# Optimization experiments

Hardware: AMD Instinct MI355X
Metric: run time of the kernel (lower is better)

## Reference

```python
import jax, jax.numpy as jnp
import numpy as np

B, S, D, R = 8, 2048, 2048, 256


def soft_threshold24(w):
    """2:4 soft-threshold: in each contiguous group of 4 along the last dim,
    keep the top-2 |w| and shrink them by the 3rd-largest |w| (soft threshold),
    zeroing the bottom two. Mirrors soft_threshold24_triton."""
    rows, K = w.shape
    g = w.reshape(rows, K // 4, 4)
    a = jnp.abs(g)
    t = jnp.sort(a, axis=-1)[..., 1:2]  # 2nd smallest == 3rd largest per group
    sp = jnp.sign(g) * jnp.maximum(a - t, 0.0)
    return sp.reshape(rows, K)


def fp16_mm(a, b):
    """fake_fp8_mm: cast operands to fp16, matmul with fp32 accumulation/output."""
    return jnp.matmul(a.astype(jnp.float16), b.astype(jnp.float16),
                      preferred_element_type=jnp.float32)


def sparse_linear(x, w, b, scale):
    """SparseOverlayFunction.forward: 2:4-sparsified, scaled weight + fp16 GEMM."""
    x2 = x.reshape(-1, x.shape[-1])                # [N, K]
    ws = soft_threshold24(w) * scale               # [K, M], 2:4 sparse * learnable scale
    out = fp16_mm(x2, ws)                          # [N, M] fp32
    out = out.reshape(x.shape[:-1] + (w.shape[-1],))
    return out + b


def setup_inputs():
    key = jax.random.key(0)
    ks = jax.random.split(key, 4)
    x = jax.random.normal(ks[0], (B, S, D), jnp.float32)
    weight_in = jax.random.normal(ks[1], (D, R), jnp.float32) * 0.02
    weight_out = jax.random.normal(ks[2], (R, D), jnp.float32) * 0.02
    bias_in = jnp.zeros((R,), jnp.float32)
    bias_out = jax.random.normal(ks[3], (D,), jnp.float32) * 0.01
    sparse_scale_in = jnp.ones((1,), jnp.float32)
    sparse_scale_out = jnp.ones((1,), jnp.float32)
    return {"x": x, "weight_in": weight_in, "weight_out": weight_out,
            "bias_in": bias_in, "bias_out": bias_out,
            "sparse_scale_in": sparse_scale_in, "sparse_scale_out": sparse_scale_out}


def reference(x, weight_in, weight_out, bias_in, bias_out, sparse_scale_in, sparse_scale_out):
    h = sparse_linear(x, weight_in, bias_in, sparse_scale_in)    # [B,S,R]
    y = sparse_linear(h, weight_out, bias_out, sparse_scale_out)  # [B,S,D]
    return y
```

## Files before the change

### kernel.cpp

```cpp
#include <hip/hip_runtime.h>
#include <stdint.h>
#include <stddef.h>

typedef _Float16 f16;
typedef __attribute__((ext_vector_type(8))) _Float16 f16x8;
typedef __attribute__((ext_vector_type(4))) float f32x4;

#define GPTR(p) ((const __attribute__((address_space(1))) void*)(p))
#define LPTR(p) ((__attribute__((address_space(3))) void*)(p))

__device__ __forceinline__ void async16(const void* g, void* l) {
    __builtin_amdgcn_global_load_lds(GPTR(g), LPTR(l), 16, 0, 0);
}

__global__ __launch_bounds__(256) void sparsify_t_tiled(
        const float* __restrict__ W, const float* __restrict__ scale,
        f16* __restrict__ Wt, int K, int M) {
    __shared__ f16 T[64][80];
    const int r0 = blockIdx.y << 6, m0 = blockIdx.x << 6;
    const float s = scale[0];
    const int t = threadIdx.x;
    const int rr = t >> 2, mb = (t & 3) << 4;
    const float* src = W + (size_t)(r0 + rr) * M + m0 + mb;
    #pragma unroll
    for (int j = 0; j < 4; j++) {
        float4 v = *(const float4*)(src + j * 4);
        float a0 = fabsf(v.x), a1 = fabsf(v.y), a2 = fabsf(v.z), a3 = fabsf(v.w);
        float lo1 = fminf(a0, a1), hi1 = fmaxf(a0, a1);
        float lo2 = fminf(a2, a3), hi2 = fmaxf(a2, a3);
        float th = fminf(fmaxf(lo1, lo2), fminf(hi1, hi2));
        int m = mb + j * 4;
        T[m + 0][rr] = (f16)(copysignf(fmaxf(a0 - th, 0.f), v.x) * s);
        T[m + 1][rr] = (f16)(copysignf(fmaxf(a1 - th, 0.f), v.y) * s);
        T[m + 2][rr] = (f16)(copysignf(fmaxf(a2 - th, 0.f), v.z) * s);
        T[m + 3][rr] = (f16)(copysignf(fmaxf(a3 - th, 0.f), v.w) * s);
    }
    __syncthreads();
    const int mm = t >> 2, rb = (t & 3) << 4;
    f16* dst = Wt + (size_t)(m0 + mm) * K + r0 + rb;
    *(f16x8*)dst       = *(const f16x8*)&T[mm][rb];
    *(f16x8*)(dst + 8) = *(const f16x8*)&T[mm][rb + 8];
}

__global__ __launch_bounds__(256, 4) void gemm1_kernel(
        const float* __restrict__ A, const f16* __restrict__ Bt,
        const float* __restrict__ bias, f16* __restrict__ H) {
    constexpr int K = 2048, RN = 256, BK = 64;
    __shared__ float4 Asf[64 * 16];
    __shared__ f16x8  Bs[64 * 8];

    const int tid  = threadIdx.x;
    const int lane = tid & 63;
    const int wv   = tid >> 6;
    const int wm   = wv & 1, wn = wv >> 1;
    const int lr   = lane & 15, q = lane >> 4;
    const int row0 = blockIdx.y << 6;
    const int col0 = blockIdx.x << 6;

    f32x4 acc[2][2] = {};

    for (int k0 = 0; k0 < K; k0 += BK) {
        #pragma unroll
        for (int j = 0; j < 4; j++) {
            int issue = wv * 4 + j;
            int L = issue * 64 + lane;
            int r = L >> 4, cp = L & 15;
            int c = (cp & 8) | ((cp & 7) ^ (r & 7));
            async16(A + (size_t)(row0 + r) * K + k0 + c * 4,
                    (char*)Asf + issue * 1024);
        }
        #pragma unroll
        for (int j = 0; j < 2; j++) {
            int issue = wv * 2 + j;
            int L = issue * 64 + lane;
            int r = L >> 3, cp = L & 7;
            int c = cp ^ (r & 7);
            async16(Bt + (size_t)(col0 + r) * K + k0 + c * 8,
                    (char*)Bs + issue * 1024);
        }
        __syncthreads();

        #pragma unroll
        for (int ks = 0; ks < 2; ks++) {
            f16x8 af[2], bf[2];
            #pragma unroll
            for (int m = 0; m < 2; m++) {
                int r = wm * 32 + m * 16 + lr;
                int c0p = ks * 8 + (((2 * q) + 0) ^ (r & 7));
                int c1p = ks * 8 + (((2 * q) + 1) ^ (r & 7));
                float4 v0 = Asf[r * 16 + c0p];
                float4 v1 = Asf[r * 16 + c1p];
                f16x8 h;
                h[0] = (f16)v0.x; h[1] = (f16)v0.y; h[2] = (f16)v0.z; h[3] = (f16)v0.w;
                h[4] = (f16)v1.x; h[5] = (f16)v1.y; h[6] = (f16)v1.z; h[7] = (f16)v1.w;
                af[m] = h;
            }
            #pragma unroll
            for (int n = 0; n < 2; n++) {
                int r = wn * 32 + n * 16 + lr;
                int cp = (ks * 4 + q) ^ (r & 7);
                bf[n] = Bs[r * 8 + cp];
            }
            #pragma unroll
            for (int m = 0; m < 2; m++)
                #pragma unroll
                for (int n = 0; n < 2; n++)
                    acc[m][n] = __builtin_amdgcn_mfma_f32_16x16x32_f16(
                        af[m], bf[n], acc[m][n], 0, 0, 0);
        }
        __syncthreads();
    }

    #pragma unroll
    for (int m = 0; m < 2; m++) {
        int gr0 = row0 + wm * 32 + m * 16 + q * 4;
        #pragma unroll
        for (int n = 0; n < 2; n++) {
            int gc = col0 + wn * 32 + n * 16 + lr;
            float bv = bias[gc];
            #pragma unroll
            for (int r = 0; r < 4; r++)
                H[(size_t)(gr0 + r) * RN + gc] = (f16)(acc[m][n][r] + bv);
        }
    }
}

__global__ __launch_bounds__(256, 4) void gemm2_kernel(
        const f16* __restrict__ H, const f16* __restrict__ Bt,
        const float* __restrict__ bias, float* __restrict__ Y) {
    constexpr int K = 256, N = 2048, BK = 64;
    __shared__ f16x8 As[64 * 8];
    __shared__ f16x8 Bs[128 * 8];

    const int tid  = threadIdx.x;
    const int lane = tid & 63;
    const int wv   = tid >> 6;
    const int wm   = wv & 1, wn = wv >> 1;
    const int lr   = lane & 15, q = lane >> 4;
    const int row0 = blockIdx.y << 6;
    const int col0 = blockIdx.x << 7;

    f32x4 acc[2][4] = {};

    for (int k0 = 0; k0 < K; k0 += BK) {
        #pragma unroll
        for (int j = 0; j < 2; j++) {
            int issue = wv * 2 + j;
            int L = issue * 64 + lane;
            int r = L >> 3, cp = L & 7;
            int c = cp ^ (r & 7);
            async16(H + (size_t)(row0 + r) * K + k0 + c * 8,
                    (char*)As + issue * 1024);
        }
        #pragma unroll
        for (int j = 0; j < 4; j++) {
            int issue = wv * 4 + j;
            int L = issue * 64 + lane;
            int r = L >> 3, cp = L & 7;
            int c = cp ^ (r & 7);
            async16(Bt + (size_t)(col0 + r) * K + k0 + c * 8,
                    (char*)Bs + issue * 1024);
        }
        __syncthreads();

        #pragma unroll
        for (int ks = 0; ks < 2; ks++) {
            f16x8 af[2], bf[4];
            #pragma unroll
            for (int m = 0; m < 2; m++) {
                int r = wm * 32 + m * 16 + lr;
                af[m] = As[r * 8 + ((ks * 4 + q) ^ (r & 7))];
            }
            #pragma unroll
            for (int n = 0; n < 4; n++) {
                int r = wn * 64 + n * 16 + lr;
                bf[n] = Bs[r * 8 + ((ks * 4 + q) ^ (r & 7))];
            }
            #pragma unroll
            for (int m = 0; m < 2; m++)
                #pragma unroll
                for (int n = 0; n < 4; n++)
                    acc[m][n] = __builtin_amdgcn_mfma_f32_16x16x32_f16(
                        af[m], bf[n], acc[m][n], 0, 0, 0);
        }
        __syncthreads();
    }

    #pragma unroll
    for (int m = 0; m < 2; m++) {
        int gr0 = row0 + wm * 32 + m * 16 + q * 4;
        #pragma unroll
        for (int n = 0; n < 4; n++) {
            int gc = col0 + wn * 64 + n * 16 + lr;
            float bv = bias[gc];
            #pragma unroll
            for (int r = 0; r < 4; r++)
                Y[(size_t)(gr0 + r) * N + gc] = acc[m][n][r] + bv;
        }
    }
}

extern "C" void kernel_launch(void* const* d_in, const int* in_sizes, int n_in,
                              void* d_out, int out_size, void* d_ws, size_t ws_size,
                              hipStream_t stream) {
    const float* x  = (const float*)d_in[0];
    const float* w1 = (const float*)d_in[1];
    const float* w2 = (const float*)d_in[2];
    const float* b1 = (const float*)d_in[3];
    const float* b2 = (const float*)d_in[4];
    const float* s1 = (const float*)d_in[5];
    const float* s2 = (const float*)d_in[6];
    float* y = (float*)d_out;

    constexpr int NROWS = 8 * 2048;
    constexpr int D = 2048, R = 256;

    char* ws = (char*)d_ws;
    f16* W1t = (f16*)ws;
    f16* W2t = (f16*)(ws + (size_t)R * D * 2);
    f16* H   = (f16*)(ws + (size_t)R * D * 4);

    hipLaunchKernelGGL(sparsify_t_tiled, dim3(R / 64, D / 64), dim3(256),
                       0, stream, w1, s1, W1t, D, R);
    hipLaunchKernelGGL(sparsify_t_tiled, dim3(D / 64, R / 64), dim3(256),
                       0, stream, w2, s2, W2t, R, D);

    hipLaunchKernelGGL(gemm1_kernel, dim3(R / 64, NROWS / 64), dim3(256),
                       0, stream, x, W1t, b1, H);

    hipLaunchKernelGGL(gemm2_kernel, dim3(D / 128, NROWS / 64), dim3(256),
                       0, stream, H, W2t, b2, y);
}
```

Measured before the change: 298.3 us.

## Double-buffer both GEMMs with 512-thread blocks and full-width N tiles

```diff
diff --git a/kernel.cpp b/kernel.cpp
--- a/kernel.cpp
+++ b/kernel.cpp
@@ -12,6 +12,11 @@
 __device__ __forceinline__ void async16(const void* g, void* l) {
     __builtin_amdgcn_global_load_lds(GPTR(g), LPTR(l), 16, 0, 0);
 }
+
+#define VMCNT(N) asm volatile("s_waitcnt vmcnt(" #N ")" ::: "memory")
+#define SBAR()   do { __builtin_amdgcn_sched_barrier(0); \
+                      __builtin_amdgcn_s_barrier();      \
+                      __builtin_amdgcn_sched_barrier(0); } while (0)
 
 __global__ __launch_bounds__(256) void sparsify_t_tiled(
         const float* __restrict__ W, const float* __restrict__ scale,
@@ -42,81 +47,82 @@
     *(f16x8*)(dst + 8) = *(const f16x8*)&T[mm][rb + 8];
 }
 
-__global__ __launch_bounds__(256, 4) void gemm1_kernel(
+__global__ __launch_bounds__(512, 2) void gemm1_kernel(
         const float* __restrict__ A, const f16* __restrict__ Bt,
         const float* __restrict__ bias, f16* __restrict__ H) {
-    constexpr int K = 2048, RN = 256, BK = 64;
-    __shared__ float4 Asf[64 * 16];
-    __shared__ f16x8  Bs[64 * 8];
+    constexpr int K = 2048, RN = 256, BK = 32, NT = K / BK;
+    __shared__ float4 Asf[2][64 * 8];
+    __shared__ f16x8  Bs[2][256 * 4];
 
     const int tid  = threadIdx.x;
     const int lane = tid & 63;
     const int wv   = tid >> 6;
     const int wm   = wv & 1, wn = wv >> 1;
     const int lr   = lane & 15, q = lane >> 4;
-    const int row0 = blockIdx.y << 6;
-    const int col0 = blockIdx.x << 6;
-
-    f32x4 acc[2][2] = {};
-
-    for (int k0 = 0; k0 < K; k0 += BK) {
-        #pragma unroll
-        for (int j = 0; j < 4; j++) {
-            int issue = wv * 4 + j;
-            int L = issue * 64 + lane;
-            int r = L >> 4, cp = L & 15;
-            int c = (cp & 8) | ((cp & 7) ^ (r & 7));
-            async16(A + (size_t)(row0 + r) * K + k0 + c * 4,
-                    (char*)Asf + issue * 1024);
-        }
-        #pragma unroll
-        for (int j = 0; j < 2; j++) {
-            int issue = wv * 2 + j;
-            int L = issue * 64 + lane;
-            int r = L >> 3, cp = L & 7;
-            int c = cp ^ (r & 7);
-            async16(Bt + (size_t)(col0 + r) * K + k0 + c * 8,
-                    (char*)Bs + issue * 1024);
-        }
-        __syncthreads();
-
-        #pragma unroll
-        for (int ks = 0; ks < 2; ks++) {
-            f16x8 af[2], bf[2];
-            #pragma unroll
-            for (int m = 0; m < 2; m++) {
-                int r = wm * 32 + m * 16 + lr;
-                int c0p = ks * 8 + (((2 * q) + 0) ^ (r & 7));
-                int c1p = ks * 8 + (((2 * q) + 1) ^ (r & 7));
-                float4 v0 = Asf[r * 16 + c0p];
-                float4 v1 = Asf[r * 16 + c1p];
-                f16x8 h;
-                h[0] = (f16)v0.x; h[1] = (f16)v0.y; h[2] = (f16)v0.z; h[3] = (f16)v0.w;
-                h[4] = (f16)v1.x; h[5] = (f16)v1.y; h[6] = (f16)v1.z; h[7] = (f16)v1.w;
-                af[m] = h;
-            }
-            #pragma unroll
-            for (int n = 0; n < 2; n++) {
-                int r = wn * 32 + n * 16 + lr;
-                int cp = (ks * 4 + q) ^ (r & 7);
-                bf[n] = Bs[r * 8 + cp];
-            }
-            #pragma unroll
-            for (int m = 0; m < 2; m++)
-                #pragma unroll
-                for (int n = 0; n < 2; n++)
-                    acc[m][n] = __builtin_amdgcn_mfma_f32_16x16x32_f16(
-                        af[m], bf[n], acc[m][n], 0, 0, 0);
-        }
-        __syncthreads();
-    }
+    const int row0 = blockIdx.x << 6;
+
+    f32x4 acc[2][4] = {};
+
+    const int La = wv * 64 + lane;
+    const int ra = La >> 3, ca = (La & 7) ^ (ra & 7);
+    const float* aSrc = A + (size_t)(row0 + ra) * K + ca * 4;
+    const int Lb0 = (wv * 2 + 0) * 64 + lane;
+    const int Lb1 = (wv * 2 + 1) * 64 + lane;
+    const int rb0 = Lb0 >> 2, cb0 = (Lb0 & 3) ^ (rb0 & 3);
+    const int rb1 = Lb1 >> 2, cb1 = (Lb1 & 3) ^ (rb1 & 3);
+    const f16* bSrc0 = Bt + (size_t)rb0 * K + cb0 * 8;
+    const f16* bSrc1 = Bt + (size_t)rb1 * K + cb1 * 8;
+
+    auto stage = [&](int k0, int b) {
+        async16(aSrc + k0,  (char*)(&Asf[b][0]) + wv * 1024);
+        async16(bSrc0 + k0, (char*)(&Bs[b][0]) + (wv * 2 + 0) * 1024);
+        async16(bSrc1 + k0, (char*)(&Bs[b][0]) + (wv * 2 + 1) * 1024);
+    };
+
+    auto compute = [&](int b) {
+        f16x8 af[2], bf[4];
+        #pragma unroll
+        for (int m = 0; m < 2; m++) {
+            int r = wm * 32 + m * 16 + lr;
+            float4 v0 = Asf[b][r * 8 + ((2 * q)     ^ (r & 7))];
+            float4 v1 = Asf[b][r * 8 + ((2 * q + 1) ^ (r & 7))];
+            f16x8 h;
+            h[0] = (f16)v0.x; h[1] = (f16)v0.y; h[2] = (f16)v0.z; h[3] = (f16)v0.w;
+            h[4] = (f16)v1.x; h[5] = (f16)v1.y; h[6] = (f16)v1.z; h[7] = (f16)v1.w;
+            af[m] = h;
+        }
+        #pragma unroll
+        for (int n = 0; n < 4; n++) {
+            int r = wn * 64 + n * 16 + lr;
+            bf[n] = Bs[b][r * 4 + (q ^ (r & 3))];
+        }
+        #pragma unroll
+        for (int m = 0; m < 2; m++)
+            #pragma unroll
+            for (int n = 0; n < 4; n++)
+                acc[m][n] = __builtin_amdgcn_mfma_f32_16x16x32_f16(
+                    af[m], bf[n], acc[m][n], 0, 0, 0);
+    };
+
+    stage(0, 0);
+    #pragma unroll 2
+    for (int t = 0; t < NT - 1; ++t) {
+        stage((t + 1) * BK, (t + 1) & 1);
+        VMCNT(3);
+        SBAR();
+        compute(t & 1);
+        SBAR();
+    }
+    VMCNT(0);
+    SBAR();
+    compute((NT - 1) & 1);
 
     #pragma unroll
     for (int m = 0; m < 2; m++) {
         int gr0 = row0 + wm * 32 + m * 16 + q * 4;
         #pragma unroll
-        for (int n = 0; n < 2; n++) {
-            int gc = col0 + wn * 32 + n * 16 + lr;
+        for (int n = 0; n < 4; n++) {
+            int gc = wn * 64 + n * 16 + lr;
             float bv = bias[gc];
             #pragma unroll
             for (int r = 0; r < 4; r++)
@@ -125,70 +131,74 @@
     }
 }
 
-__global__ __launch_bounds__(256, 4) void gemm2_kernel(
-        const f16* __restrict__ H, const f16* __restrict__ Bt,
+__global__ __launch_bounds__(512, 2) void gemm2_kernel(
+        const f16* __restrict__ Hs, const f16* __restrict__ Bt,
         const float* __restrict__ bias, float* __restrict__ Y) {
-    constexpr int K = 256, N = 2048, BK = 64;
-    __shared__ f16x8 As[64 * 8];
-    __shared__ f16x8 Bs[128 * 8];
+    constexpr int K = 256, N = 2048, BK = 32, NT = K / BK;
+    __shared__ f16x8 As[2][128 * 4];
+    __shared__ f16x8 Bs[2][256 * 4];
 
     const int tid  = threadIdx.x;
     const int lane = tid & 63;
     const int wv   = tid >> 6;
     const int wm   = wv & 1, wn = wv >> 1;
     const int lr   = lane & 15, q = lane >> 4;
-    const int row0 = blockIdx.y << 6;
-    const int col0 = blockIdx.x << 7;
-
-    f32x4 acc[2][4] = {};
-
-    for (int k0 = 0; k0 < K; k0 += BK) {
-        #pragma unroll
-        for (int j = 0; j < 2; j++) {
-            int issue = wv * 2 + j;
-            int L = issue * 64 + lane;
-            int r = L >> 3, cp = L & 7;
-            int c = cp ^ (r & 7);
-            async16(H + (size_t)(row0 + r) * K + k0 + c * 8,
-                    (char*)As + issue * 1024);
-        }
-        #pragma unroll
-        for (int j = 0; j < 4; j++) {
-            int issue = wv * 4 + j;
-            int L = issue * 64 + lane;
-            int r = L >> 3, cp = L & 7;
-            int c = cp ^ (r & 7);
-            async16(Bt + (size_t)(col0 + r) * K + k0 + c * 8,
-                    (char*)Bs + issue * 1024);
-        }
-        __syncthreads();
-
-        #pragma unroll
-        for (int ks = 0; ks < 2; ks++) {
-            f16x8 af[2], bf[4];
-            #pragma unroll
-            for (int m = 0; m < 2; m++) {
-                int r = wm * 32 + m * 16 + lr;
-                af[m] = As[r * 8 + ((ks * 4 + q) ^ (r & 7))];
-            }
-            #pragma unroll
-            for (int n = 0; n < 4; n++) {
-                int r = wn * 64 + n * 16 + lr;
-                bf[n] = Bs[r * 8 + ((ks * 4 + q) ^ (r & 7))];
-            }
-            #pragma unroll
-            for (int m = 0; m < 2; m++)
-                #pragma unroll
-                for (int n = 0; n < 4; n++)
-                    acc[m][n] = __builtin_amdgcn_mfma_f32_16x16x32_f16(
-                        af[m], bf[n], acc[m][n], 0, 0, 0);
-        }
-        __syncthreads();
-    }
+    const int row0 = blockIdx.y << 7;
+    const int col0 = blockIdx.x << 8;
+
+    f32x4 acc[4][4] = {};
+
+    const int La = wv * 64 + lane;
+    const int ra = La >> 2, ca = (La & 3) ^ (ra & 3);
+    const f16* aSrc = Hs + (size_t)(row0 + ra) * K + ca * 8;
+    const int Lb0 = (wv * 2 + 0) * 64 + lane;
+    const int Lb1 = (wv * 2 + 1) * 64 + lane;
+    const int rb0 = Lb0 >> 2, cb0 = (Lb0 & 3) ^ (rb0 & 3);
+    const int rb1 = Lb1 >> 2, cb1 = (Lb1 & 3) ^ (rb1 & 3);
+    const f16* bSrc0 = Bt + (size_t)(col0 + rb0) * K + cb0 * 8;
+    const f16* bSrc1 = Bt + (size_t)(col0 + rb1) * K + cb1 * 8;
+
+    auto stage = [&](int k0, int b) {
+        async16(aSrc + k0,  (char*)(&As[b][0]) + wv * 1024);
+        async16(bSrc0 + k0, (char*)(&Bs[b][0]) + (wv * 2 + 0) * 1024);
+        async16(bSrc1 + k0, (char*)(&Bs[b][0]) + (wv * 2 + 1) * 1024);
+    };
+
+    auto compute = [&](int b) {
+        f16x8 af[4], bf[4];
+        #pragma unroll
+        for (int m = 0; m < 4; m++) {
+            int r = wm * 64 + m * 16 + lr;
+            af[m] = As[b][r * 4 + (q ^ (r & 3))];
+        }
+        #pragma unroll
+        for (int n = 0; n < 4; n++) {
+            int r = wn * 64 + n * 16 + lr;
+            bf[n] = Bs[b][r * 4 + (q ^ (r & 3))];
+        }
+        #pragma unroll
+        for (int m = 0; m < 4; m++)
+            #pragma unroll
+            for (int n = 0; n < 4; n++)
+                acc[m][n] = __builtin_amdgcn_mfma_f32_16x16x32_f16(
+                    af[m], bf[n], acc[m][n], 0, 0, 0);
+    };
+
+    stage(0, 0);
+    for (int t = 0; t < NT - 1; ++t) {
+        stage((t + 1) * BK, (t + 1) & 1);
+        VMCNT(3);
+        SBAR();
+        compute(t & 1);
+        SBAR();
+    }
+    VMCNT(0);
+    SBAR();
+    compute((NT - 1) & 1);
 
     #pragma unroll
-    for (int m = 0; m < 2; m++) {
-        int gr0 = row0 + wm * 32 + m * 16 + q * 4;
+    for (int m = 0; m < 4; m++) {
+        int gr0 = row0 + wm * 64 + m * 16 + q * 4;
         #pragma unroll
         for (int n = 0; n < 4; n++) {
             int gc = col0 + wn * 64 + n * 16 + lr;
@@ -225,9 +235,9 @@
     hipLaunchKernelGGL(sparsify_t_tiled, dim3(D / 64, R / 64), dim3(256),
                        0, stream, w2, s2, W2t, R, D);
 
-    hipLaunchKernelGGL(gemm1_kernel, dim3(R / 64, NROWS / 64), dim3(256),
+    hipLaunchKernelGGL(gemm1_kernel, dim3(NROWS / 64), dim3(512),
                        0, stream, x, W1t, b1, H);
 
-    hipLaunchKernelGGL(gemm2_kernel, dim3(D / 128, NROWS / 64), dim3(256),
+    hipLaunchKernelGGL(gemm2_kernel, dim3(D / 256, NROWS / 128), dim3(512),
                        0, stream, H, W2t, b2, y);
 }
```

Measured after the change: 298.6 us. Within noise of the previous version (+0.1%).

## Store weights and hidden activations in MFMA fragment-native layout with swizzled block order

Applied to the files above, without the earlier changes.

```diff
diff --git a/kernel.cpp b/kernel.cpp
--- a/kernel.cpp
+++ b/kernel.cpp
@@ -13,9 +13,9 @@
     __builtin_amdgcn_global_load_lds(GPTR(g), LPTR(l), 16, 0, 0);
 }
 
-__global__ __launch_bounds__(256) void sparsify_t_tiled(
+__global__ __launch_bounds__(256) void sparsify_frag(
         const float* __restrict__ W, const float* __restrict__ scale,
-        f16* __restrict__ Wt, int K, int M) {
+        f16* __restrict__ Wf, int K, int M) {
     __shared__ f16 T[64][80];
     const int r0 = blockIdx.y << 6, m0 = blockIdx.x << 6;
     const float s = scale[0];
@@ -37,70 +37,82 @@
     }
     __syncthreads();
     const int mm = t >> 2, rb = (t & 3) << 4;
-    f16* dst = Wt + (size_t)(m0 + mm) * K + r0 + rb;
-    *(f16x8*)dst       = *(const f16x8*)&T[mm][rb];
-    *(f16x8*)(dst + 8) = *(const f16x8*)&T[mm][rb + 8];
+    const int col = m0 + mm;
+    const int Mb = M >> 4;
+    #pragma unroll
+    for (int h = 0; h < 2; h++) {
+        int k = r0 + rb + h * 8;
+        size_t blk = ((size_t)(k >> 5) * Mb + (col >> 4)) * 64
+                   + (size_t)(((k >> 3) & 3) * 16 + (col & 15));
+        *(f16x8*)(Wf + blk * 8) = *(const f16x8*)&T[mm][rb + h * 8];
+    }
 }
 
 __global__ __launch_bounds__(256, 4) void gemm1_kernel(
-        const float* __restrict__ A, const f16* __restrict__ Bt,
-        const float* __restrict__ bias, f16* __restrict__ H) {
-    constexpr int K = 2048, RN = 256, BK = 64;
+        const float* __restrict__ A, const f16* __restrict__ Bf,
+        const float* __restrict__ bias, f16* __restrict__ Hf) {
+    constexpr int K = 2048, BK = 64, NT = K / BK;
     __shared__ float4 Asf[64 * 16];
-    __shared__ f16x8  Bs[64 * 8];
-
-    const int tid  = threadIdx.x;
-    const int lane = tid & 63;
-    const int wv   = tid >> 6;
-    const int wm   = wv & 1, wn = wv >> 1;
-    const int lr   = lane & 15, q = lane >> 4;
-    const int row0 = blockIdx.y << 6;
-    const int col0 = blockIdx.x << 6;
+    __shared__ f16x8  Bs[8 * 64];
+
+    const int tid = threadIdx.x, lane = tid & 63, wv = tid >> 6;
+    const int wm = wv & 1, wn = wv >> 1;
+    const int lr = lane & 15, q = lane >> 4;
+
+    const int id = blockIdx.x + (blockIdx.y << 2);
+    const int xr = id & 7, xt = id >> 3;
+    const int nb = xt & 3, p = xr + ((xt >> 2) << 3);
+    const int row0 = p << 6, col0 = nb << 6;
 
     f32x4 acc[2][2] = {};
 
-    for (int k0 = 0; k0 < K; k0 += BK) {
+    const float* aSrc[4];
+    #pragma unroll
+    for (int j = 0; j < 4; j++) {
+        int i = wv * 4 + j;
+        int r = i * 4 + (lane >> 4);
+        int c = lane & 15;
+        int cs = (c & 8) | ((c & 7) ^ (r & 7));
+        aSrc[j] = A + (size_t)(row0 + r) * K + cs * 4;
+    }
+    const f16* bSrc[2];
+    #pragma unroll
+    for (int j = 0; j < 2; j++) {
+        int ch = wv * 2 + j;
+        int s = ch >> 2, c = ch & 3;
+        bSrc[j] = Bf + (((size_t)s * 16 + (col0 >> 4) + c) * 64) * 8 + lane * 8;
+    }
+
+    for (int t = 0; t < NT; ++t) {
         #pragma unroll
         for (int j = 0; j < 4; j++) {
-            int issue = wv * 4 + j;
-            int L = issue * 64 + lane;
-            int r = L >> 4, cp = L & 15;
-            int c = (cp & 8) | ((cp & 7) ^ (r & 7));
-            async16(A + (size_t)(row0 + r) * K + k0 + c * 4,
-                    (char*)Asf + issue * 1024);
+            int i = wv * 4 + j;
+            async16(aSrc[j], (char*)Asf + i * 1024);
+            aSrc[j] += BK;
         }
         #pragma unroll
         for (int j = 0; j < 2; j++) {
-            int issue = wv * 2 + j;
-            int L = issue * 64 + lane;
-            int r = L >> 3, cp = L & 7;
-            int c = cp ^ (r & 7);
-            async16(Bt + (size_t)(col0 + r) * K + k0 + c * 8,
-                    (char*)Bs + issue * 1024);
-        }
-        __syncthreads();
-
+            int ch = wv * 2 + j;
+            async16(bSrc[j], (char*)Bs + ch * 1024);
+            bSrc[j] += 2 * 16 * 64 * 8;
+        }
+        __syncthreads();
         #pragma unroll
         for (int ks = 0; ks < 2; ks++) {
             f16x8 af[2], bf[2];
             #pragma unroll
             for (int m = 0; m < 2; m++) {
                 int r = wm * 32 + m * 16 + lr;
-                int c0p = ks * 8 + (((2 * q) + 0) ^ (r & 7));
-                int c1p = ks * 8 + (((2 * q) + 1) ^ (r & 7));
-                float4 v0 = Asf[r * 16 + c0p];
-                float4 v1 = Asf[r * 16 + c1p];
+                float4 v0 = Asf[r * 16 + (ks * 8 + ((2 * q)     ^ (r & 7)))];
+                float4 v1 = Asf[r * 16 + (ks * 8 + ((2 * q + 1) ^ (r & 7)))];
                 f16x8 h;
                 h[0] = (f16)v0.x; h[1] = (f16)v0.y; h[2] = (f16)v0.z; h[3] = (f16)v0.w;
                 h[4] = (f16)v1.x; h[5] = (f16)v1.y; h[6] = (f16)v1.z; h[7] = (f16)v1.w;
                 af[m] = h;
             }
             #pragma unroll
-            for (int n = 0; n < 2; n++) {
-                int r = wn * 32 + n * 16 + lr;
-                int cp = (ks * 4 + q) ^ (r & 7);
-                bf[n] = Bs[r * 8 + cp];
-            }
+            for (int n = 0; n < 2; n++)
+                bf[n] = Bs[(ks * 4 + wn * 2 + n) * 64 + lane];
             #pragma unroll
             for (int m = 0; m < 2; m++)
                 #pragma unroll
@@ -113,73 +125,70 @@
 
     #pragma unroll
     for (int m = 0; m < 2; m++) {
-        int gr0 = row0 + wm * 32 + m * 16 + q * 4;
+        int r16 = (row0 + wm * 32 + m * 16) >> 4;
         #pragma unroll
         for (int n = 0; n < 2; n++) {
             int gc = col0 + wn * 32 + n * 16 + lr;
             float bv = bias[gc];
-            #pragma unroll
-            for (int r = 0; r < 4; r++)
-                H[(size_t)(gr0 + r) * RN + gc] = (f16)(acc[m][n][r] + bv);
+            int kt = gc >> 5, qq = (gc >> 3) & 3, e = gc & 7;
+            f16* hb = Hf + ((((size_t)kt * 1024 + r16) * 4 + qq) * 16) * 8 + e;
+            #pragma unroll
+            for (int rr = 0; rr < 4; rr++)
+                hb[(q * 4 + rr) * 8] = (f16)(acc[m][n][rr] + bv);
         }
     }
 }
 
 __global__ __launch_bounds__(256, 4) void gemm2_kernel(
-        const f16* __restrict__ H, const f16* __restrict__ Bt,
+        const f16* __restrict__ Hf, const f16* __restrict__ Bf,
         const float* __restrict__ bias, float* __restrict__ Y) {
-    constexpr int K = 256, N = 2048, BK = 64;
-    __shared__ f16x8 As[64 * 8];
-    __shared__ f16x8 Bs[128 * 8];
-
-    const int tid  = threadIdx.x;
-    const int lane = tid & 63;
-    const int wv   = tid >> 6;
-    const int wm   = wv & 1, wn = wv >> 1;
-    const int lr   = lane & 15, q = lane >> 4;
-    const int row0 = blockIdx.y << 6;
-    const int col0 = blockIdx.x << 7;
-
-    f32x4 acc[2][4] = {};
-
-    for (int k0 = 0; k0 < K; k0 += BK) {
+    constexpr int N = 2048, NT = 4;
+    __shared__ f16x8 As[16 * 64];
+    __shared__ f16x8 Bs[8 * 64];
+
+    const int tid = threadIdx.x, lane = tid & 63, wv = tid >> 6;
+    const int wm = wv & 1, wn = wv >> 1;
+    const int lr = lane & 15, q = lane >> 4;
+
+    const int id = blockIdx.x + (blockIdx.y << 5);
+    const int xr = id & 7, xt = id >> 3;
+    const int bx = xt & 31, by = xr + ((xt >> 5) << 3);
+    const int row0 = by << 7, col0 = bx << 6;
+
+    f32x4 acc[4][2] = {};
+
+    for (int t = 0; t < NT; ++t) {
+        int kt0 = 2 * t;
+        #pragma unroll
+        for (int j = 0; j < 4; j++) {
+            int i = wv * 4 + j;
+            int s = i >> 3, rb = i & 7;
+            const f16* srcp = Hf + (((size_t)(kt0 + s) * 1024 + (row0 >> 4) + rb) * 64) * 8
+                              + lane * 8;
+            async16(srcp, (char*)As + i * 1024);
+        }
         #pragma unroll
         for (int j = 0; j < 2; j++) {
-            int issue = wv * 2 + j;
-            int L = issue * 64 + lane;
-            int r = L >> 3, cp = L & 7;
-            int c = cp ^ (r & 7);
-            async16(H + (size_t)(row0 + r) * K + k0 + c * 8,
-                    (char*)As + issue * 1024);
-        }
-        #pragma unroll
-        for (int j = 0; j < 4; j++) {
-            int issue = wv * 4 + j;
-            int L = issue * 64 + lane;
-            int r = L >> 3, cp = L & 7;
-            int c = cp ^ (r & 7);
-            async16(Bt + (size_t)(col0 + r) * K + k0 + c * 8,
-                    (char*)Bs + issue * 1024);
-        }
-        __syncthreads();
-
+            int ch = wv * 2 + j;
+            int s = ch >> 2, c = ch & 3;
+            const f16* srcp = Bf + (((size_t)(kt0 + s) * 128 + (col0 >> 4) + c) * 64) * 8
+                              + lane * 8;
+            async16(srcp, (char*)Bs + ch * 1024);
+        }
+        __syncthreads();
         #pragma unroll
         for (int ks = 0; ks < 2; ks++) {
-            f16x8 af[2], bf[4];
-            #pragma unroll
-            for (int m = 0; m < 2; m++) {
-                int r = wm * 32 + m * 16 + lr;
-                af[m] = As[r * 8 + ((ks * 4 + q) ^ (r & 7))];
-            }
-            #pragma unroll
-            for (int n = 0; n < 4; n++) {
-                int r = wn * 64 + n * 16 + lr;
-                bf[n] = Bs[r * 8 + ((ks * 4 + q) ^ (r & 7))];
-            }
-            #pragma unroll
-            for (int m = 0; m < 2; m++)
+            f16x8 af[4], bf[2];
+            #pragma unroll
+            for (int m = 0; m < 4; m++)
+                af[m] = As[(ks * 8 + wm * 4 + m) * 64 + lane];
+            #pragma unroll
+            for (int n = 0; n < 2; n++)
+                bf[n] = Bs[(ks * 4 + wn * 2 + n) * 64 + lane];
+            #pragma unroll
+            for (int m = 0; m < 4; m++)
                 #pragma unroll
-                for (int n = 0; n < 4; n++)
+                for (int n = 0; n < 2; n++)
                     acc[m][n] = __builtin_amdgcn_mfma_f32_16x16x32_f16(
                         af[m], bf[n], acc[m][n], 0, 0, 0);
         }
@@ -187,15 +196,15 @@
     }
 
     #pragma unroll
-    for (int m = 0; m < 2; m++) {
-        int gr0 = row0 + wm * 32 + m * 16 + q * 4;
-        #pragma unroll
-        for (int n = 0; n < 4; n++) {
-            int gc = col0 + wn * 64 + n * 16 + lr;
+    for (int m = 0; m < 4; m++) {
+        int gr0 = row0 + wm * 64 + m * 16 + q * 4;
+        #pragma unroll
+        for (int n = 0; n < 2; n++) {
+            int gc = col0 + wn * 32 + n * 16 + lr;
             float bv = bias[gc];
             #pragma unroll
-            for (int r = 0; r < 4; r++)
-                Y[(size_t)(gr0 + r) * N + gc] = acc[m][n][r] + bv;
+            for (int rr = 0; rr < 4; rr++)
+                Y[(size_t)(gr0 + rr) * N + gc] = acc[m][n][rr] + bv;
         }
     }
 }
@@ -216,18 +225,18 @@
     constexpr int D = 2048, R = 256;
 
     char* ws = (char*)d_ws;
-    f16* W1t = (f16*)ws;
-    f16* W2t = (f16*)(ws + (size_t)R * D * 2);
-    f16* H   = (f16*)(ws + (size_t)R * D * 4);
-
-    hipLaunchKernelGGL(sparsify_t_tiled, dim3(R / 64, D / 64), dim3(256),
-                       0, stream, w1, s1, W1t, D, R);
-    hipLaunchKernelGGL(sparsify_t_tiled, dim3(D / 64, R / 64), dim3(256),
-                       0, stream, w2, s2, W2t, R, D);
-
-    hipLaunchKernelGGL(gemm1_kernel, dim3(R / 64, NROWS / 64), dim3(256),
-                       0, stream, x, W1t, b1, H);
-
-    hipLaunchKernelGGL(gemm2_kernel, dim3(D / 128, NROWS / 64), dim3(256),
-                       0, stream, H, W2t, b2, y);
-}
+    f16* W1f = (f16*)ws;
+    f16* W2f = (f16*)(ws + (2u << 20));
+    f16* Hf  = (f16*)(ws + (4u << 20));
+
+    hipLaunchKernelGGL(sparsify_frag, dim3(R / 64, D / 64), dim3(256),
+                       0, stream, w1, s1, W1f, D, R);
+    hipLaunchKernelGGL(sparsify_frag, dim3(D / 64, R / 64), dim3(256),
+                       0, stream, w2, s2, W2f, R, D);
+
+    hipLaunchKernelGGL(gemm1_kernel, dim3(4, NROWS / 64), dim3(256),
+                       0, stream, x, W1f, b1, Hf);
+
+    hipLaunchKernelGGL(gemm2_kernel, dim3(D / 64, NROWS / 128), dim3(256),
+                       0, stream, Hf, W2f, b2, y);
+}
```

Result: faster. 290.7 us (-2.5%).
